# Kernel tuning notes

Hardware: AMD Instinct MI355X
Metric: run time of the kernel (lower is better)

The kernel has to match this reference:

```python
import jax, jax.numpy as jnp
import numpy as np

# ---- constants reconstructing the DMC lookup tables (topology_to_triangles, x/y/z, inner) ----
GRID = 32            # cells per axis -> offset grid is (GRID+1)^3
T = 48               # number of triangle-bearing topologies
MAXTRI = 4           # max triangles per topology (marching cubes)
EPS = 1e-8

# 12 marching-cubes edges of a cell: (corner offset dx,dy,dz, axis of edge)
EDGES = [(0,0,0,0),(1,0,0,1),(0,1,0,0),(0,0,0,1),
         (0,0,1,0),(1,0,1,1),(0,1,1,0),(0,0,1,1),
         (0,0,0,2),(1,0,0,2),(1,1,0,2),(0,1,0,2)]

# Deterministic stand-in for the MC triangle table: per topology, up to 4 triangles,
# each triangle = 3 edge indices in [0,12). TRI_MASK marks valid triangles.
_rs = np.random.RandomState(0)
TRI_TABLE = jnp.asarray(_rs.randint(0, 12, (T, MAXTRI, 3)))          # [T,4,3] int
_ntri = _rs.randint(1, MAXTRI + 1, (T,))
TRI_MASK = jnp.asarray((np.arange(MAXTRI)[None, :] < _ntri[:, None]).astype(np.float32))  # [T,4]


def _edge_vertices(offset):
    """offset: [3, G, G, G] -> per-cell edge vertex positions [N_cells, 12, 3].
    Vertex on an edge = edge midpoint + scalar offset along the edge axis."""
    ci = jnp.arange(GRID)
    I, J, K = jnp.meshgrid(ci, ci, ci, indexing='ij')  # [32,32,32]
    verts = []
    for (dx, dy, dz, a) in EDGES:  # fixed small loop over 12 edges
        gi, gj, gk = I + dx, J + dy, K + dz
        base = jnp.stack([gi, gj, gk], axis=-1).astype(offset.dtype)  # [32,32,32,3]
        disp = offset[a, gi, gj, gk]                                   # [32,32,32]
        unit = jnp.zeros((3,), offset.dtype).at[a].set(1.0)
        verts.append(base + (0.5 + disp)[..., None] * unit)
    V = jnp.stack(verts, axis=3)          # [32,32,32,12,3]
    return V.reshape(-1, 12, 3)            # [N,12,3]


def setup_inputs() -> dict:
    key = jax.random.key(0)
    k0, k1 = jax.random.split(key)
    offset = jax.random.normal(k0, (3, GRID + 1, GRID + 1, GRID + 1), dtype=jnp.float32)
    topology = jax.random.uniform(k1, (GRID ** 3, T), dtype=jnp.float32)
    return {"offset": offset, "topology": topology}


def reference(offset, topology):
    V = _edge_vertices(offset)                  # [N,12,3]
    tv = V[:, TRI_TABLE]                        # [N,T,4,3verts,3]  (irregular gather)
    # unnormalized face normals, then normalize
    n = jnp.cross(tv[..., 1, :] - tv[..., 0, :], tv[..., 2, :] - tv[..., 0, :])  # [N,T,4,3]
    n = n / (jnp.linalg.norm(n, axis=-1, keepdims=True) + EPS)

    # within-cell curvature: squared normal difference of consecutive triangle pairs
    d = n[:, :, 1:, :] - n[:, :, :-1, :]        # [N,T,3,3]
    pair_mask = TRI_MASK[:, 1:] * TRI_MASK[:, :-1]  # [T,3]
    within = jnp.einsum('ntpc,tp->nt', d * d, pair_mask)
    loss_within = jnp.einsum('nt,nt->', topology, within)

    # cross-cell curvature between adjacent cells (the 'inner' pair term),
    # factored so no [N,T,T] tensor is materialized:
    # sum_{t1,t2} p1 p2 ||m1-m2||^2 = s1*P2 + s2*P1 - 2 e1.e2
    cnt = TRI_MASK.sum(-1)                                   # [T]
    m = jnp.einsum('ntpc,tp->ntc', n, TRI_MASK) / cnt[None, :, None]  # mean normal [N,T,3]
    e = jnp.einsum('nt,ntc->nc', topology, m)                # [N,3]
    s = jnp.einsum('nt,nt->n', topology, (m * m).sum(-1))    # [N]
    P = topology.sum(-1)                                      # [N]
    G3 = (GRID, GRID, GRID)
    e3 = e.reshape(*G3, 3)
    s3 = s.reshape(G3)
    P3 = P.reshape(G3)
    loss_cross = jnp.zeros((), offset.dtype)
    for ax in range(3):
        ea = jnp.moveaxis(e3, ax, 0); sa = jnp.moveaxis(s3, ax, 0); pa = jnp.moveaxis(P3, ax, 0)
        e_l, e_r = ea[:-1], ea[1:]
        s_l, s_r = sa[:-1], sa[1:]
        p_l, p_r = pa[:-1], pa[1:]
        loss_cross = loss_cross + (s_l * p_r + s_r * p_l - 2.0 * (e_l * e_r).sum(-1)).sum()
    return (loss_within + loss_cross).reshape(1)
```

## Files before the change

kernel.cpp:

```cpp
#include <hip/hip_runtime.h>
#include <hip/hip_cooperative_groups.h>

namespace cg = cooperative_groups;

namespace {

constexpr int T = 48;
constexpr int MAXTRI = 4;
constexpr int NCELLS = 32 * 32 * 32;
constexpr float EPSF = 1e-8f;
constexpr int NBLK = NCELLS / 64;
constexpr int NBLK_CROSS = NCELLS / 256;
constexpr int NWAVE = 8;

struct Tables {
  int tri[T][MAXTRI][3];
  int ntri[T];
};

struct MT {
  unsigned mt[624];
  int pos;
  constexpr MT() : mt{}, pos(624) {
    unsigned s = 0u;
    for (int i = 0; i < 624; ++i) {
      mt[i] = s;
      s = 1812433253u * (s ^ (s >> 30)) + (unsigned)(i + 1);
    }
  }
  constexpr unsigned next() {
    if (pos == 624) {
      for (int i = 0; i < 624; ++i) {
        unsigned y = (mt[i] & 0x80000000u) | (mt[(i + 1) % 624] & 0x7fffffffu);
        unsigned v = mt[(i + 397) % 624] ^ (y >> 1);
        if (y & 1u) v ^= 0x9908b0dfu;
        mt[i] = v;
      }
      pos = 0;
    }
    unsigned y = mt[pos++];
    y ^= y >> 11;
    y ^= (y << 7) & 0x9d2c5680u;
    y ^= (y << 15) & 0xefc60000u;
    y ^= y >> 18;
    return y;
  }
  constexpr unsigned draw(unsigned mask, unsigned rng) {
    unsigned v = next() & mask;
    while (v > rng) v = next() & mask;
    return v;
  }
};

constexpr Tables make_tables() {
  Tables tb{};
  MT g{};
  for (int t = 0; t < T; ++t)
    for (int p = 0; p < MAXTRI; ++p)
      for (int c = 0; c < 3; ++c)
        tb.tri[t][p][c] = (int)g.draw(15u, 11u);
  for (int t = 0; t < T; ++t)
    tb.ntri[t] = 1 + (int)g.draw(3u, 3u);
  return tb;
}

constexpr Tables TB = make_tables();

struct Splits { int s[NWAVE + 1]; };
constexpr Splits make_splits() {
  Splits sp{};
  int total = 0;
  for (int t = 0; t < T; ++t) total += 3 * TB.ntri[t] + 2;
  sp.s[0] = 0;
  int acc = 0, t = 0;
  for (int w = 1; w < NWAVE; ++w) {
    const int target = (total * w + NWAVE / 2) / NWAVE;
    while (t < T && acc < target) { acc += 3 * TB.ntri[t] + 2; ++t; }
    sp.s[w] = t;
  }
  sp.s[NWAVE] = T;
  return sp;
}
constexpr Splits SP = make_splits();

constexpr int EDX[12] = {0,1,0,0,0,1,0,0,0,1,1,0};
constexpr int EDY[12] = {0,0,1,0,0,0,1,0,0,0,1,1};
constexpr int EDZ[12] = {0,0,0,0,1,1,1,1,0,0,0,0};
constexpr int EAX[12] = {0,1,0,1,0,1,0,1,2,2,2,2};

template <int t, int p>
__device__ __forceinline__ void tri_normals(const float (&vx)[12], const float (&vy)[12],
                                            const float (&vz)[12], float (&nx)[MAXTRI],
                                            float (&ny)[MAXTRI], float (&nz)[MAXTRI]) {
  if constexpr (p < TB.ntri[t]) {
    constexpr int e0 = TB.tri[t][p][0];
    constexpr int e1 = TB.tri[t][p][1];
    constexpr int e2 = TB.tri[t][p][2];
    float ax = vx[e1] - vx[e0], ay = vy[e1] - vy[e0], az = vz[e1] - vz[e0];
    float bx = vx[e2] - vx[e0], by = vy[e2] - vy[e0], bz = vz[e2] - vz[e0];
    float cx = ay * bz - az * by;
    float cy = az * bx - ax * bz;
    float cz = ax * by - ay * bx;
    float nrm = __builtin_amdgcn_sqrtf(cx * cx + cy * cy + cz * cz);
    float inv = __builtin_amdgcn_rcpf(nrm + EPSF);
    nx[p] = cx * inv; ny[p] = cy * inv; nz[p] = cz * inv;
    tri_normals<t, p + 1>(vx, vy, vz, nx, ny, nz);
  }
}

template <int t>
__device__ __forceinline__ void accum_t(const float (&vx)[12], const float (&vy)[12],
                                        const float (&vz)[12], float tv, float& lw, float& ex,
                                        float& ey, float& ez, float& ss, float& pp) {
  constexpr int nt = TB.ntri[t];
  float nx[MAXTRI] = {0.f, 0.f, 0.f, 0.f};
  float ny[MAXTRI] = {0.f, 0.f, 0.f, 0.f};
  float nz[MAXTRI] = {0.f, 0.f, 0.f, 0.f};
  tri_normals<t, 0>(vx, vy, vz, nx, ny, nz);

  float within = 0.f;
  if constexpr (nt > 1) {
    float dx = nx[1] - nx[0], dy = ny[1] - ny[0], dz = nz[1] - nz[0];
    within += dx * dx + dy * dy + dz * dz;
  }
  if constexpr (nt > 2) {
    float dx = nx[2] - nx[1], dy = ny[2] - ny[1], dz = nz[2] - nz[1];
    within += dx * dx + dy * dy + dz * dz;
  }
  if constexpr (nt > 3) {
    float dx = nx[3] - nx[2], dy = ny[3] - ny[2], dz = nz[3] - nz[2];
    within += dx * dx + dy * dy + dz * dz;
  }

  float mx = nx[0], my = ny[0], mz = nz[0];
  if constexpr (nt > 1) { mx += nx[1]; my += ny[1]; mz += nz[1]; }
  if constexpr (nt > 2) { mx += nx[2]; my += ny[2]; mz += nz[2]; }
  if constexpr (nt > 3) { mx += nx[3]; my += ny[3]; mz += nz[3]; }
  constexpr float invn = 1.0f / (float)nt;
  mx *= invn; my *= invn; mz *= invn;

  lw += tv * within;
  ex += tv * mx; ey += tv * my; ez += tv * mz;
  ss += tv * (mx * mx + my * my + mz * mz);
  pp += tv;
}

template <int t0, int t1>
__device__ __forceinline__ void accum_range(const float (&vx)[12], const float (&vy)[12],
                                            const float (&vz)[12], const float* s_topo, int lane,
                                            float& lw, float& ex, float& ey, float& ez, float& ss,
                                            float& pp) {
  if constexpr (t0 < t1) {
    float tv = s_topo[t0 * 64 + lane];
    accum_t<t0>(vx, vy, vz, tv, lw, ex, ey, ez, ss, pp);
    accum_range<t0 + 1, t1>(vx, vy, vz, s_topo, lane, lw, ex, ey, ez, ss, pp);
  }
}

__device__ __forceinline__ void phase1(const float* __restrict__ offset,
                                       const float* __restrict__ topo,
                                       const float* s_topo, int wid, int lane, int cell0,
                                       float& lw, float& ex, float& ey, float& ez, float& ss,
                                       float& pp) {
  const int n = cell0 + lane;
  const int i = n >> 10, j = (n >> 5) & 31, k = n & 31;

  float vx[12], vy[12], vz[12];
#pragma unroll
  for (int e = 0; e < 12; ++e) {
    const int gi = i + EDX[e], gj = j + EDY[e], gk = k + EDZ[e];
    const int a = EAX[e];
    const float disp = offset[a * 35937 + gi * 1089 + gj * 33 + gk];
    float px = (float)gi, py = (float)gj, pz = (float)gk;
    const float d = 0.5f + disp;
    if (a == 0) px += d; else if (a == 1) py += d; else pz += d;
    vx[e] = px; vy[e] = py; vz[e] = pz;
  }

  switch (wid) {
    case 0:  accum_range<SP.s[0], SP.s[1]>(vx, vy, vz, s_topo, lane, lw, ex, ey, ez, ss, pp); break;
    case 1:  accum_range<SP.s[1], SP.s[2]>(vx, vy, vz, s_topo, lane, lw, ex, ey, ez, ss, pp); break;
    case 2:  accum_range<SP.s[2], SP.s[3]>(vx, vy, vz, s_topo, lane, lw, ex, ey, ez, ss, pp); break;
    case 3:  accum_range<SP.s[3], SP.s[4]>(vx, vy, vz, s_topo, lane, lw, ex, ey, ez, ss, pp); break;
    case 4:  accum_range<SP.s[4], SP.s[5]>(vx, vy, vz, s_topo, lane, lw, ex, ey, ez, ss, pp); break;
    case 5:  accum_range<SP.s[5], SP.s[6]>(vx, vy, vz, s_topo, lane, lw, ex, ey, ez, ss, pp); break;
    case 6:  accum_range<SP.s[6], SP.s[7]>(vx, vy, vz, s_topo, lane, lw, ex, ey, ez, ss, pp); break;
    default: accum_range<SP.s[7], SP.s[8]>(vx, vy, vz, s_topo, lane, lw, ex, ey, ez, ss, pp); break;
  }
}

__device__ __forceinline__ void stage_topo(const float* __restrict__ topo, float* s_topo,
                                           int tid, int cell0) {
  const float4* g4 = reinterpret_cast<const float4*>(topo + (size_t)cell0 * T);
#pragma unroll
  for (int it = 0; it < 2; ++it) {
    int idx = tid + it * 512;
    if (idx < 768) {
      float4 v = g4[idx];
      int cell = idx / 12;
      int tq = (idx % 12) * 4;
      s_topo[(tq + 0) * 64 + cell] = v.x;
      s_topo[(tq + 1) * 64 + cell] = v.y;
      s_topo[(tq + 2) * 64 + cell] = v.z;
      s_topo[(tq + 3) * 64 + cell] = v.w;
    }
  }
}

__device__ __forceinline__ float cross_for_cell(const float* __restrict__ wsE,
                                                const float* __restrict__ wsS,
                                                const float* __restrict__ wsP, int n) {
  const int i = n >> 10, j = (n >> 5) & 31, k = n & 31;
  const float* ex = wsE;
  const float* ey = wsE + NCELLS;
  const float* ez = wsE + 2 * NCELLS;
  const float sl = wsS[n], pl = wsP[n];
  const float exl = ex[n], eyl = ey[n], ezl = ez[n];
  float acc = 0.f;
  if (i < 31) {
    int r = n + 1024;
    acc += sl * wsP[r] + wsS[r] * pl - 2.f * (exl * ex[r] + eyl * ey[r] + ezl * ez[r]);
  }
  if (j < 31) {
    int r = n + 32;
    acc += sl * wsP[r] + wsS[r] * pl - 2.f * (exl * ex[r] + eyl * ey[r] + ezl * ez[r]);
  }
  if (k < 31) {
    int r = n + 1;
    acc += sl * wsP[r] + wsS[r] * pl - 2.f * (exl * ex[r] + eyl * ey[r] + ezl * ez[r]);
  }
  return acc;
}

__global__ __launch_bounds__(512, 4) void fused_kernel(const float* __restrict__ offset,
                                                       const float* __restrict__ topo,
                                                       float* __restrict__ wsE,
                                                       float* __restrict__ wsS,
                                                       float* __restrict__ wsP,
                                                       float* __restrict__ wsACC,
                                                       int* __restrict__ wsTicket,
                                                       float* __restrict__ out) {
  __shared__ float s_topo[T * 64];
  __shared__ float s_part[6][NWAVE][64];
  __shared__ float s_lw;
  const int tid = threadIdx.x;
  const int lane = tid & 63;
  const int wid = tid >> 6;
  const int cell0 = blockIdx.x * 64;

  if (blockIdx.x == 0 && tid == 0) {
    atomicExch(wsACC, 0.0f);
    atomicExch(wsTicket, 0);
  }

  stage_topo(topo, s_topo, tid, cell0);
  __syncthreads();

  {
    float lw = 0.f, ex = 0.f, ey = 0.f, ez = 0.f, ss = 0.f, pp = 0.f;
    phase1(offset, topo, s_topo, wid, lane, cell0, lw, ex, ey, ez, ss, pp);
    s_part[0][wid][lane] = ex;
    s_part[1][wid][lane] = ey;
    s_part[2][wid][lane] = ez;
    s_part[3][wid][lane] = ss;
    s_part[4][wid][lane] = pp;
    s_part[5][wid][lane] = lw;
  }
  __syncthreads();

  if (tid < 384) {
    const int q = tid >> 6, c = tid & 63;
    float v = 0.f;
#pragma unroll
    for (int w = 0; w < NWAVE; ++w) v += s_part[q][w][c];
    const int nn = cell0 + c;
    if (q == 0) wsE[nn] = v;
    else if (q == 1) wsE[NCELLS + nn] = v;
    else if (q == 2) wsE[2 * NCELLS + nn] = v;
    else if (q == 3) wsS[nn] = v;
    else if (q == 4) wsP[nn] = v;
    else {
#pragma unroll
      for (int off = 32; off > 0; off >>= 1) v += __shfl_down(v, off);
      if (c == 0) s_lw = v;
    }
  }

  cg::this_grid().sync();

  if (tid < 64) {
    float acc = cross_for_cell(wsE, wsS, wsP, cell0 + tid);
#pragma unroll
    for (int off = 32; off > 0; off >>= 1) acc += __shfl_down(acc, off);

    if (tid == 0) {
      atomicAdd(wsACC, acc + s_lw);
      __threadfence();
      int old = atomicAdd(wsTicket, 1);
      if (old == NBLK - 1) {
        out[0] = atomicAdd(wsACC, 0.0f);
      }
    }
  }
}

__global__ __launch_bounds__(512) void cell_kernel(const float* __restrict__ offset,
                                                   const float* __restrict__ topo,
                                                   float* __restrict__ wsE,
                                                   float* __restrict__ wsS,
                                                   float* __restrict__ wsP,
                                                   float* __restrict__ wsLW,
                                                   float* __restrict__ wsACC,
                                                   int* __restrict__ wsTicket) {
  __shared__ float s_topo[T * 64];
  __shared__ float s_part[6][NWAVE][64];
  const int tid = threadIdx.x;
  const int lane = tid & 63;
  const int wid = tid >> 6;
  const int cell0 = blockIdx.x * 64;

  if (blockIdx.x == 0 && tid == 0) {
    atomicExch(wsACC, 0.0f);
    atomicExch(wsTicket, 0);
  }

  stage_topo(topo, s_topo, tid, cell0);
  __syncthreads();

  {
    float lw = 0.f, ex = 0.f, ey = 0.f, ez = 0.f, ss = 0.f, pp = 0.f;
    phase1(offset, topo, s_topo, wid, lane, cell0, lw, ex, ey, ez, ss, pp);
    s_part[0][wid][lane] = ex;
    s_part[1][wid][lane] = ey;
    s_part[2][wid][lane] = ez;
    s_part[3][wid][lane] = ss;
    s_part[4][wid][lane] = pp;
    s_part[5][wid][lane] = lw;
  }
  __syncthreads();

  if (tid < 384) {
    const int q = tid >> 6, c = tid & 63;
    float v = 0.f;
#pragma unroll
    for (int w = 0; w < NWAVE; ++w) v += s_part[q][w][c];
    const int nn = cell0 + c;
    if (q == 0) wsE[nn] = v;
    else if (q == 1) wsE[NCELLS + nn] = v;
    else if (q == 2) wsE[2 * NCELLS + nn] = v;
    else if (q == 3) wsS[nn] = v;
    else if (q == 4) wsP[nn] = v;
    else {
#pragma unroll
      for (int off = 32; off > 0; off >>= 1) v += __shfl_down(v, off);
      if (c == 0) wsLW[blockIdx.x] = v;
    }
  }
}

__global__ __launch_bounds__(256) void cross_kernel(const float* __restrict__ wsE,
                                                    const float* __restrict__ wsS,
                                                    const float* __restrict__ wsP,
                                                    const float* __restrict__ wsLW,
                                                    float* __restrict__ wsACC,
                                                    int* __restrict__ wsTicket,
                                                    float* __restrict__ out) {
  const int n = blockIdx.x * 256 + threadIdx.x;
  float acc = cross_for_cell(wsE, wsS, wsP, n);

#pragma unroll
  for (int off = 32; off > 0; off >>= 1) acc += __shfl_down(acc, off);
  __shared__ float wpart[4];
  __shared__ int s_last;
  const int lane = threadIdx.x & 63, w = threadIdx.x >> 6;
  if (lane == 0) wpart[w] = acc;
  __syncthreads();

  if (threadIdx.x == 0) {
    float bsum = wpart[0] + wpart[1] + wpart[2] + wpart[3];
    atomicAdd(wsACC, bsum);
    __threadfence();
    int old = atomicAdd(wsTicket, 1);
    s_last = (old == NBLK_CROSS - 1) ? 1 : 0;
  }
  __syncthreads();

  if (s_last) {
    float v = 0.f;
#pragma unroll
    for (int it = 0; it < NBLK / 256; ++it) v += wsLW[threadIdx.x + it * 256];
#pragma unroll
    for (int off = 32; off > 0; off >>= 1) v += __shfl_down(v, off);
    if (lane == 0) wpart[w] = v;
    __syncthreads();
    if (threadIdx.x == 0) {
      float cross = atomicAdd(wsACC, 0.0f);
      out[0] = cross + wpart[0] + wpart[1] + wpart[2] + wpart[3];
    }
  }
}

}

extern "C" void kernel_launch(void* const* d_in, const int* in_sizes, int n_in,
                              void* d_out, int out_size, void* d_ws, size_t ws_size,
                              hipStream_t stream) {
  const float* offset = (const float*)d_in[0];
  const float* topo = (const float*)d_in[1];
  float* out = (float*)d_out;
  float* wsE = (float*)d_ws;
  float* wsS = wsE + 3 * NCELLS;
  float* wsP = wsS + NCELLS;
  float* wsLW = wsP + NCELLS;
  float* wsACC = wsLW + NBLK;
  int* wsTicket = (int*)(wsACC + 1);

  int dev = 0;
  hipGetDevice(&dev);
  int coop = 0, nCU = 0, maxBlk = 0;
  hipDeviceGetAttribute(&coop, hipDeviceAttributeCooperativeLaunch, dev);
  hipDeviceGetAttribute(&nCU, hipDeviceAttributeMultiprocessorCount, dev);
  hipOccupancyMaxActiveBlocksPerMultiprocessor(&maxBlk, fused_kernel, 512, 0);

  if (coop && (long)maxBlk * nCU >= NBLK) {
    void* args[] = {(void*)&offset, (void*)&topo, (void*)&wsE, (void*)&wsS,
                    (void*)&wsP, (void*)&wsACC, (void*)&wsTicket, (void*)&out};
    hipError_t err = hipLaunchCooperativeKernel((const void*)fused_kernel, dim3(NBLK),
                                                dim3(512), args, 0, stream);
    if (err == hipSuccess) return;
  }

  hipLaunchKernelGGL(cell_kernel, dim3(NBLK), dim3(512), 0, stream,
                     offset, topo, wsE, wsS, wsP, wsLW, wsACC, wsTicket);
  hipLaunchKernelGGL(cross_kernel, dim3(NBLK_CROSS), dim3(256), 0, stream,
                     wsE, wsS, wsP, wsLW, wsACC, wsTicket, out);
}
```

Baseline: 18.29 us.

## Stage edge vertices in LDS, pad tiles, and replace atomic reduction with grid-sync

Edge vertex positions are now computed once per block cooperatively and staged in padded shared memory, instead of every wave recomputing all 12 gathers per cell. The topology tile gets a padded stride of 65 to avoid LDS bank conflicts. The cross-cell term reuses in-block neighbours from shared memory rather than global memory. The final atomic-plus-ticket reduction is replaced by per-block partials and a second grid sync with block 0 summing. The second grid barrier adds synchronisation cost, and the extra LDS may lower occupancy.

New measurement: 20.97 us. +14.6%, slower.

```diff
diff --git a/kernel.cpp b/kernel.cpp
--- a/kernel.cpp
+++ b/kernel.cpp
@@ -12,6 +12,7 @@
 constexpr int NBLK = NCELLS / 64;
 constexpr int NBLK_CROSS = NCELLS / 256;
 constexpr int NWAVE = 8;
+constexpr int TP = 65;
 
 struct Tables {
   int tri[T][MAXTRI][3];
@@ -151,32 +152,17 @@
                                             float& lw, float& ex, float& ey, float& ez, float& ss,
                                             float& pp) {
   if constexpr (t0 < t1) {
-    float tv = s_topo[t0 * 64 + lane];
+    float tv = s_topo[t0 * TP + lane];
     accum_t<t0>(vx, vy, vz, tv, lw, ex, ey, ez, ss, pp);
     accum_range<t0 + 1, t1>(vx, vy, vz, s_topo, lane, lw, ex, ey, ez, ss, pp);
   }
 }
 
-__device__ __forceinline__ void phase1(const float* __restrict__ offset,
-                                       const float* __restrict__ topo,
-                                       const float* s_topo, int wid, int lane, int cell0,
-                                       float& lw, float& ex, float& ey, float& ez, float& ss,
-                                       float& pp) {
-  const int n = cell0 + lane;
-  const int i = n >> 10, j = (n >> 5) & 31, k = n & 31;
-
-  float vx[12], vy[12], vz[12];
-#pragma unroll
-  for (int e = 0; e < 12; ++e) {
-    const int gi = i + EDX[e], gj = j + EDY[e], gk = k + EDZ[e];
-    const int a = EAX[e];
-    const float disp = offset[a * 35937 + gi * 1089 + gj * 33 + gk];
-    float px = (float)gi, py = (float)gj, pz = (float)gk;
-    const float d = 0.5f + disp;
-    if (a == 0) px += d; else if (a == 1) py += d; else pz += d;
-    vx[e] = px; vy[e] = py; vz[e] = pz;
-  }
-
+__device__ __forceinline__ void accum_dispatch(int wid, const float (&vx)[12],
+                                               const float (&vy)[12], const float (&vz)[12],
+                                               const float* s_topo, int lane, float& lw,
+                                               float& ex, float& ey, float& ez, float& ss,
+                                               float& pp) {
   switch (wid) {
     case 0:  accum_range<SP.s[0], SP.s[1]>(vx, vy, vz, s_topo, lane, lw, ex, ey, ez, ss, pp); break;
     case 1:  accum_range<SP.s[1], SP.s[2]>(vx, vy, vz, s_topo, lane, lw, ex, ey, ez, ss, pp); break;
@@ -189,47 +175,41 @@
   }
 }
 
-__device__ __forceinline__ void stage_topo(const float* __restrict__ topo, float* s_topo,
-                                           int tid, int cell0) {
+__device__ __forceinline__ void stage_block(const float* __restrict__ offset,
+                                            const float* __restrict__ topo,
+                                            float* s_topo, float* s_vert,
+                                            int tid, int cell0) {
   const float4* g4 = reinterpret_cast<const float4*>(topo + (size_t)cell0 * T);
 #pragma unroll
   for (int it = 0; it < 2; ++it) {
     int idx = tid + it * 512;
     if (idx < 768) {
       float4 v = g4[idx];
-      int cell = idx / 12;
-      int tq = (idx % 12) * 4;
-      s_topo[(tq + 0) * 64 + cell] = v.x;
-      s_topo[(tq + 1) * 64 + cell] = v.y;
-      s_topo[(tq + 2) * 64 + cell] = v.z;
-      s_topo[(tq + 3) * 64 + cell] = v.w;
-    }
-  }
-}
-
-__device__ __forceinline__ float cross_for_cell(const float* __restrict__ wsE,
-                                                const float* __restrict__ wsS,
-                                                const float* __restrict__ wsP, int n) {
-  const int i = n >> 10, j = (n >> 5) & 31, k = n & 31;
-  const float* ex = wsE;
-  const float* ey = wsE + NCELLS;
-  const float* ez = wsE + 2 * NCELLS;
-  const float sl = wsS[n], pl = wsP[n];
-  const float exl = ex[n], eyl = ey[n], ezl = ez[n];
-  float acc = 0.f;
-  if (i < 31) {
-    int r = n + 1024;
-    acc += sl * wsP[r] + wsS[r] * pl - 2.f * (exl * ex[r] + eyl * ey[r] + ezl * ez[r]);
-  }
-  if (j < 31) {
-    int r = n + 32;
-    acc += sl * wsP[r] + wsS[r] * pl - 2.f * (exl * ex[r] + eyl * ey[r] + ezl * ez[r]);
-  }
-  if (k < 31) {
-    int r = n + 1;
-    acc += sl * wsP[r] + wsS[r] * pl - 2.f * (exl * ex[r] + eyl * ey[r] + ezl * ez[r]);
-  }
-  return acc;
+      int cell = idx / 12, tq = (idx % 12) * 4;
+      s_topo[(tq + 0) * TP + cell] = v.x;
+      s_topo[(tq + 1) * TP + cell] = v.y;
+      s_topo[(tq + 2) * TP + cell] = v.z;
+      s_topo[(tq + 3) * TP + cell] = v.w;
+    }
+  }
+#pragma unroll
+  for (int it = 0; it < 2; ++it) {
+    int u = tid + it * 512;
+    if (u < 768) {
+      int e = u >> 6, cell = u & 63;
+      int n = cell0 + cell;
+      int i = n >> 10, j = (n >> 5) & 31, k = n & 31;
+      int gi = i + EDX[e], gj = j + EDY[e], gk = k + EDZ[e];
+      int a = EAX[e];
+      float disp = offset[a * 35937 + gi * 1089 + gj * 33 + gk];
+      float px = (float)gi, py = (float)gj, pz = (float)gk;
+      float d = 0.5f + disp;
+      if (a == 0) px += d; else if (a == 1) py += d; else pz += d;
+      s_vert[e * TP + cell] = px;
+      s_vert[(12 + e) * TP + cell] = py;
+      s_vert[(24 + e) * TP + cell] = pz;
+    }
+  }
 }
 
 __global__ __launch_bounds__(512, 4) void fused_kernel(const float* __restrict__ offset,
@@ -237,15 +217,120 @@
                                                        float* __restrict__ wsE,
                                                        float* __restrict__ wsS,
                                                        float* __restrict__ wsP,
-                                                       float* __restrict__ wsACC,
-                                                       int* __restrict__ wsTicket,
+                                                       float* __restrict__ wsPart,
                                                        float* __restrict__ out) {
-  __shared__ float s_topo[T * 64];
+  __shared__ float s_topo[T * TP];
+  __shared__ float s_vert[36 * TP];
   __shared__ float s_part[6][NWAVE][64];
+  __shared__ float s_esp[5][64];
   __shared__ float s_lw;
-  const int tid = threadIdx.x;
-  const int lane = tid & 63;
-  const int wid = tid >> 6;
+  __shared__ float s_fin[8];
+  const int tid = threadIdx.x, lane = tid & 63, wid = tid >> 6;
+  const int cell0 = blockIdx.x * 64;
+
+  stage_block(offset, topo, s_topo, s_vert, tid, cell0);
+  __syncthreads();
+
+  {
+    float vx[12], vy[12], vz[12];
+#pragma unroll
+    for (int e = 0; e < 12; ++e) {
+      vx[e] = s_vert[e * TP + lane];
+      vy[e] = s_vert[(12 + e) * TP + lane];
+      vz[e] = s_vert[(24 + e) * TP + lane];
+    }
+    float lw = 0.f, ex = 0.f, ey = 0.f, ez = 0.f, ss = 0.f, pp = 0.f;
+    accum_dispatch(wid, vx, vy, vz, s_topo, lane, lw, ex, ey, ez, ss, pp);
+    s_part[0][wid][lane] = ex;
+    s_part[1][wid][lane] = ey;
+    s_part[2][wid][lane] = ez;
+    s_part[3][wid][lane] = ss;
+    s_part[4][wid][lane] = pp;
+    s_part[5][wid][lane] = lw;
+  }
+  __syncthreads();
+
+  if (tid < 384) {
+    const int q = tid >> 6, c = tid & 63;
+    float v = 0.f;
+#pragma unroll
+    for (int w = 0; w < NWAVE; ++w) v += s_part[q][w][c];
+    const int nn = cell0 + c;
+    if (q == 0) { wsE[nn] = v; s_esp[0][c] = v; }
+    else if (q == 1) { wsE[NCELLS + nn] = v; s_esp[1][c] = v; }
+    else if (q == 2) { wsE[2 * NCELLS + nn] = v; s_esp[2][c] = v; }
+    else if (q == 3) { wsS[nn] = v; s_esp[3][c] = v; }
+    else if (q == 4) { wsP[nn] = v; s_esp[4][c] = v; }
+    else {
+#pragma unroll
+      for (int off = 32; off > 0; off >>= 1) v += __shfl_down(v, off);
+      if (c == 0) s_lw = v;
+    }
+  }
+
+  cg::this_grid().sync();
+
+  if (tid < 64) {
+    const int n = cell0 + tid;
+    const int i = n >> 10, j = (n >> 5) & 31, k = n & 31;
+    const float exl = s_esp[0][tid], eyl = s_esp[1][tid], ezl = s_esp[2][tid];
+    const float sl = s_esp[3][tid], pl = s_esp[4][tid];
+    float acc = 0.f;
+    if (i < 31) {
+      int r = n + 1024;
+      acc += sl * wsP[r] + wsS[r] * pl -
+             2.f * (exl * wsE[r] + eyl * wsE[NCELLS + r] + ezl * wsE[2 * NCELLS + r]);
+    }
+    if (j < 31) {
+      if (tid < 32) {
+        int r = tid + 32;
+        acc += sl * s_esp[4][r] + s_esp[3][r] * pl -
+               2.f * (exl * s_esp[0][r] + eyl * s_esp[1][r] + ezl * s_esp[2][r]);
+      } else {
+        int r = n + 32;
+        acc += sl * wsP[r] + wsS[r] * pl -
+               2.f * (exl * wsE[r] + eyl * wsE[NCELLS + r] + ezl * wsE[2 * NCELLS + r]);
+      }
+    }
+    if (k < 31) {
+      int r = tid + 1;
+      acc += sl * s_esp[4][r] + s_esp[3][r] * pl -
+             2.f * (exl * s_esp[0][r] + eyl * s_esp[1][r] + ezl * s_esp[2][r]);
+    }
+#pragma unroll
+    for (int off = 32; off > 0; off >>= 1) acc += __shfl_down(acc, off);
+    if (tid == 0) wsPart[blockIdx.x] = acc + s_lw;
+  }
+
+  cg::this_grid().sync();
+
+  if (blockIdx.x == 0) {
+    float v = wsPart[tid];
+#pragma unroll
+    for (int off = 32; off > 0; off >>= 1) v += __shfl_down(v, off);
+    if (lane == 0) s_fin[wid] = v;
+    __syncthreads();
+    if (tid == 0) {
+      float s = 0.f;
+#pragma unroll
+      for (int w = 0; w < 8; ++w) s += s_fin[w];
+      out[0] = s;
+    }
+  }
+}
+
+__global__ __launch_bounds__(512) void cell_kernel(const float* __restrict__ offset,
+                                                   const float* __restrict__ topo,
+                                                   float* __restrict__ wsE,
+                                                   float* __restrict__ wsS,
+                                                   float* __restrict__ wsP,
+                                                   float* __restrict__ wsLW,
+                                                   float* __restrict__ wsACC,
+                                                   int* __restrict__ wsTicket) {
+  __shared__ float s_topo[T * TP];
+  __shared__ float s_vert[36 * TP];
+  __shared__ float s_part[6][NWAVE][64];
+  const int tid = threadIdx.x, lane = tid & 63, wid = tid >> 6;
   const int cell0 = blockIdx.x * 64;
 
   if (blockIdx.x == 0 && tid == 0) {
@@ -253,12 +338,19 @@
     atomicExch(wsTicket, 0);
   }
 
-  stage_topo(topo, s_topo, tid, cell0);
+  stage_block(offset, topo, s_topo, s_vert, tid, cell0);
   __syncthreads();
 
   {
+    float vx[12], vy[12], vz[12];
+#pragma unroll
+    for (int e = 0; e < 12; ++e) {
+      vx[e] = s_vert[e * TP + lane];
+      vy[e] = s_vert[(12 + e) * TP + lane];
+      vz[e] = s_vert[(24 + e) * TP + lane];
+    }
     float lw = 0.f, ex = 0.f, ey = 0.f, ez = 0.f, ss = 0.f, pp = 0.f;
-    phase1(offset, topo, s_topo, wid, lane, cell0, lw, ex, ey, ez, ss, pp);
+    accum_dispatch(wid, vx, vy, vz, s_topo, lane, lw, ex, ey, ez, ss, pp);
     s_part[0][wid][lane] = ex;
     s_part[1][wid][lane] = ey;
     s_part[2][wid][lane] = ez;
@@ -282,77 +374,6 @@
     else {
 #pragma unroll
       for (int off = 32; off > 0; off >>= 1) v += __shfl_down(v, off);
-      if (c == 0) s_lw = v;
-    }
-  }
-
-  cg::this_grid().sync();
-
-  if (tid < 64) {
-    float acc = cross_for_cell(wsE, wsS, wsP, cell0 + tid);
-#pragma unroll
-    for (int off = 32; off > 0; off >>= 1) acc += __shfl_down(acc, off);
-
-    if (tid == 0) {
-      atomicAdd(wsACC, acc + s_lw);
-      __threadfence();
-      int old = atomicAdd(wsTicket, 1);
-      if (old == NBLK - 1) {
-        out[0] = atomicAdd(wsACC, 0.0f);
-      }
-    }
-  }
-}
-
-__global__ __launch_bounds__(512) void cell_kernel(const float* __restrict__ offset,
-                                                   const float* __restrict__ topo,
-                                                   float* __restrict__ wsE,
-                                                   float* __restrict__ wsS,
-                                                   float* __restrict__ wsP,
-                                                   float* __restrict__ wsLW,
-                                                   float* __restrict__ wsACC,
-                                                   int* __restrict__ wsTicket) {
-  __shared__ float s_topo[T * 64];
-  __shared__ float s_part[6][NWAVE][64];
-  const int tid = threadIdx.x;
-  const int lane = tid & 63;
-  const int wid = tid >> 6;
-  const int cell0 = blockIdx.x * 64;
-
-  if (blockIdx.x == 0 && tid == 0) {
-    atomicExch(wsACC, 0.0f);
-    atomicExch(wsTicket, 0);
-  }
-
-  stage_topo(topo, s_topo, tid, cell0);
-  __syncthreads();
-
-  {
-    float lw = 0.f, ex = 0.f, ey = 0.f, ez = 0.f, ss = 0.f, pp = 0.f;
-    phase1(offset, topo, s_topo, wid, lane, cell0, lw, ex, ey, ez, ss, pp);
-    s_part[0][wid][lane] = ex;
-    s_part[1][wid][lane] = ey;
-    s_part[2][wid][lane] = ez;
-    s_part[3][wid][lane] = ss;
-    s_part[4][wid][lane] = pp;
-    s_part[5][wid][lane] = lw;
-  }
-  __syncthreads();
-
-  if (tid < 384) {
-    const int q = tid >> 6, c = tid & 63;
-    float v = 0.f;
-#pragma unroll
-    for (int w = 0; w < NWAVE; ++w) v += s_part[q][w][c];
-    const int nn = cell0 + c;
-    if (q == 0) wsE[nn] = v;
-    else if (q == 1) wsE[NCELLS + nn] = v;
-    else if (q == 2) wsE[2 * NCELLS + nn] = v;
-    else if (q == 3) wsS[nn] = v;
-    else if (q == 4) wsP[nn] = v;
-    else {
-#pragma unroll
-      for (int off = 32; off > 0; off >>= 1) v += __shfl_down(v, off);
       if (c == 0) wsLW[blockIdx.x] = v;
     }
   }
@@ -366,7 +387,25 @@
                                                     int* __restrict__ wsTicket,
                                                     float* __restrict__ out) {
   const int n = blockIdx.x * 256 + threadIdx.x;
-  float acc = cross_for_cell(wsE, wsS, wsP, n);
+  const int i = n >> 10, j = (n >> 5) & 31, k = n & 31;
+  const float sl = wsS[n], pl = wsP[n];
+  const float exl = wsE[n], eyl = wsE[NCELLS + n], ezl = wsE[2 * NCELLS + n];
+  float acc = 0.f;
+  if (i < 31) {
+    int r = n + 1024;
+    acc += sl * wsP[r] + wsS[r] * pl -
+           2.f * (exl * wsE[r] + eyl * wsE[NCELLS + r] + ezl * wsE[2 * NCELLS + r]);
+  }
+  if (j < 31) {
+    int r = n + 32;
+    acc += sl * wsP[r] + wsS[r] * pl -
+           2.f * (exl * wsE[r] + eyl * wsE[NCELLS + r] + ezl * wsE[2 * NCELLS + r]);
+  }
+  if (k < 31) {
+    int r = n + 1;
+    acc += sl * wsP[r] + wsS[r] * pl -
+           2.f * (exl * wsE[r] + eyl * wsE[NCELLS + r] + ezl * wsE[2 * NCELLS + r]);
+  }
 
 #pragma unroll
   for (int off = 32; off > 0; off >>= 1) acc += __shfl_down(acc, off);
@@ -411,7 +450,8 @@
   float* wsE = (float*)d_ws;
   float* wsS = wsE + 3 * NCELLS;
   float* wsP = wsS + NCELLS;
-  float* wsLW = wsP + NCELLS;
+  float* wsPart = wsP + NCELLS;
+  float* wsLW = wsPart + NBLK;
   float* wsACC = wsLW + NBLK;
   int* wsTicket = (int*)(wsACC + 1);
 
@@ -424,7 +464,7 @@
 
   if (coop && (long)maxBlk * nCU >= NBLK) {
     void* args[] = {(void*)&offset, (void*)&topo, (void*)&wsE, (void*)&wsS,
-                    (void*)&wsP, (void*)&wsACC, (void*)&wsTicket, (void*)&out};
+                    (void*)&wsP, (void*)&wsPart, (void*)&out};
     hipError_t err = hipLaunchCooperativeKernel((const void*)fused_kernel, dim3(NBLK),
                                                 dim3(512), args, 0, stream);
     if (err == hipSuccess) return;
```
